# Performance work log

Measured on AMD Instinct MI355X. Metric: run time of the kernel, lower is better.

The kernel has to match this reference:

```python
import jax, jax.numpy as jnp
import numpy as np

B, N, C, K = 2, 4096, 256, 64


def setup_inputs() -> dict:
    key = jax.random.key(0)
    k1, k2, k3, k4, k5, k6 = jax.random.split(key, 6)
    points = jax.random.normal(k1, (B, N, 3), dtype=jnp.float32)  # ~N(0,1) cloud
    point_features = jax.random.normal(k2, (B, N, C), dtype=jnp.float32)
    # proposals: centers inside the cloud, positive box dims, random yaw (unused by mask math)
    centers = jax.random.uniform(k3, (B, K, 3), minval=-1.0, maxval=1.0, dtype=jnp.float32)
    dims = jax.random.uniform(k4, (B, K, 3), minval=0.5, maxval=1.5, dtype=jnp.float32)
    ry = jax.random.uniform(k5, (B, K, 1), minval=-np.pi, maxval=np.pi, dtype=jnp.float32)
    proposals = jnp.concatenate([centers, dims, ry], axis=-1)  # (B,K,7)
    W1 = jax.random.normal(k6, (C, 256), dtype=jnp.float32) * (1.0 / np.sqrt(C))
    b1 = jnp.zeros((256,), dtype=jnp.float32)
    W2 = jax.random.normal(jax.random.fold_in(key, 7), (256, 256), dtype=jnp.float32) * (1.0 / 16.0)
    b2 = jnp.zeros((256,), dtype=jnp.float32)
    return {"points": points, "point_features": point_features, "proposals": proposals,
            "W1": W1, "b1": b1, "W2": W2, "b2": b2}


def reference(points, point_features, proposals, W1, b1, W2, b2):
    # points: (B,N,3), point_features: (B,N,C), proposals: (B,K,7)
    ctr = proposals[..., :3]                      # (B,K,3) cx,cy,cz
    half = proposals[..., 3:6] * 0.5              # (B,K,3) l/2,w/2,h/2
    lo = ctr - half                               # (B,K,3)
    hi = ctr + half
    # point-in-box mask (axis-aligned, strict inequalities as in source): (B,K,N)
    p = points[:, None, :, :]                     # (B,1,N,3)
    mask = jnp.all((p > lo[:, :, None, :]) & (p < hi[:, :, None, :]), axis=-1)
    any_in = jnp.any(mask, axis=-1)               # (B,K)
    # masked max-pool over points: (B,K,N,C) -> (B,K,C)
    neg_inf = jnp.asarray(-jnp.inf, point_features.dtype)
    masked = jnp.where(mask[..., None], point_features[:, None, :, :], neg_inf)
    pooled = jnp.max(masked, axis=2)
    pooled = jnp.where(any_in[..., None], pooled, 0.0)  # empty box -> zeros
    # fc: Linear(C,256) + ReLU + Linear(256,256) + ReLU
    h = jax.nn.relu(jnp.einsum('bkc,cd->bkd', pooled, W1) + b1)
    out = jax.nn.relu(jnp.einsum('bkd,de->bke', h, W2) + b2)
    return out
```

## Files before the change

kernel.cpp:

```cpp
#include <hip/hip_runtime.h>

#define Bn 2
#define Nn 4096
#define Cn 256
#define Kn 64
#define BK (Bn * Kn)
#define NW 16
#define BT 1024

__device__ __forceinline__ float4 max4(float4 a, float4 b) {
    return make_float4(fmaxf(a.x, b.x), fmaxf(a.y, b.y),
                       fmaxf(a.z, b.z), fmaxf(a.w, b.w));
}

__global__ __launch_bounds__(BT) void fused_roi_kernel(
    const float* __restrict__ points,
    const float* __restrict__ feats,
    const float* __restrict__ proposals,
    const float* __restrict__ W1,
    const float* __restrict__ b1,
    const float* __restrict__ W2,
    const float* __restrict__ b2,
    float* __restrict__ out)
{
    const int bk   = blockIdx.x;
    const int b    = bk / Kn;
    const int tid  = threadIdx.x;
    const int w    = tid >> 6;
    const int lane = tid & 63;

    __shared__ int   s_idx[Nn];
    __shared__ int   s_count;
    __shared__ float s_part[NW][Cn];
    __shared__ float s_vec[Cn];
    __shared__ float s_red[4][Cn];

    const float* prop = proposals + (size_t)bk * 7;
    const float cx = prop[0], cy = prop[1], cz = prop[2];
    const float hx = prop[3] * 0.5f, hy = prop[4] * 0.5f, hz = prop[5] * 0.5f;
    const float lox = cx - hx, loy = cy - hy, loz = cz - hz;
    const float hix = cx + hx, hiy = cy + hy, hiz = cz + hz;

    if (tid == 0) s_count = 0;
    __syncthreads();

    const float* pts = points + (size_t)b * Nn * 3;
    #pragma unroll
    for (int n = tid; n < Nn; n += BT) {
        const float px = pts[n * 3 + 0];
        const float py = pts[n * 3 + 1];
        const float pz = pts[n * 3 + 2];
        const bool in = (px > lox) & (px < hix) &
                        (py > loy) & (py < hiy) &
                        (pz > loz) & (pz < hiz);
        if (in) {
            const int pos = atomicAdd(&s_count, 1);
            s_idx[pos] = n;
        }
    }
    __syncthreads();
    const int count = s_count;

    const float* fb = feats + (size_t)b * Nn * Cn;
    float4 mx = make_float4(-INFINITY, -INFINITY, -INFINITY, -INFINITY);
    int i = w;
    for (; i + 7 * NW < count; i += 8 * NW) {
        const int a0 = s_idx[i + 0 * NW], a1 = s_idx[i + 1 * NW];
        const int a2 = s_idx[i + 2 * NW], a3 = s_idx[i + 3 * NW];
        const int a4 = s_idx[i + 4 * NW], a5 = s_idx[i + 5 * NW];
        const int a6 = s_idx[i + 6 * NW], a7 = s_idx[i + 7 * NW];
        const float4 f0 = *(const float4*)(fb + (size_t)a0 * Cn + lane * 4);
        const float4 f1 = *(const float4*)(fb + (size_t)a1 * Cn + lane * 4);
        const float4 f2 = *(const float4*)(fb + (size_t)a2 * Cn + lane * 4);
        const float4 f3 = *(const float4*)(fb + (size_t)a3 * Cn + lane * 4);
        const float4 f4 = *(const float4*)(fb + (size_t)a4 * Cn + lane * 4);
        const float4 f5 = *(const float4*)(fb + (size_t)a5 * Cn + lane * 4);
        const float4 f6 = *(const float4*)(fb + (size_t)a6 * Cn + lane * 4);
        const float4 f7 = *(const float4*)(fb + (size_t)a7 * Cn + lane * 4);
        mx = max4(mx, max4(max4(f0, f1), max4(f2, f3)));
        mx = max4(mx, max4(max4(f4, f5), max4(f6, f7)));
    }
    for (; i < count; i += NW) {
        const int a = s_idx[i];
        mx = max4(mx, *(const float4*)(fb + (size_t)a * Cn + lane * 4));
    }
    *(float4*)&s_part[w][lane * 4] = mx;
    __syncthreads();

    if (tid < Cn) {
        float m = s_part[0][tid];
        #pragma unroll
        for (int k = 1; k < NW; ++k) m = fmaxf(m, s_part[k][tid]);
        if (m == -INFINITY) m = 0.0f;
        s_vec[tid] = m;
    }
    __syncthreads();

    {
        const int g = tid >> 8;
        const int d = tid & 255;
        const float* w1 = W1 + (size_t)(g * 64) * 256 + d;
        const float* sv = s_vec + g * 64;
        float acc = 0.0f;
        #pragma unroll 16
        for (int c = 0; c < 64; ++c) {
            acc = fmaf(sv[c], w1[(size_t)c * 256], acc);
        }
        s_red[g][d] = acc;
    }
    __syncthreads();
    if (tid < Cn) {
        const float h = fmaxf(
            b1[tid] + ((s_red[0][tid] + s_red[1][tid]) +
                       (s_red[2][tid] + s_red[3][tid])), 0.0f);
        s_vec[tid] = h;
    }
    __syncthreads();

    {
        const int g = tid >> 8;
        const int d = tid & 255;
        const float* w2 = W2 + (size_t)(g * 64) * 256 + d;
        const float* sv = s_vec + g * 64;
        float acc = 0.0f;
        #pragma unroll 16
        for (int c = 0; c < 64; ++c) {
            acc = fmaf(sv[c], w2[(size_t)c * 256], acc);
        }
        s_red[g][d] = acc;
    }
    __syncthreads();
    if (tid < Cn) {
        out[(size_t)bk * 256 + tid] = fmaxf(
            b2[tid] + ((s_red[0][tid] + s_red[1][tid]) +
                       (s_red[2][tid] + s_red[3][tid])), 0.0f);
    }
}

extern "C" void kernel_launch(void* const* d_in, const int* in_sizes, int n_in,
                              void* d_out, int out_size, void* d_ws, size_t ws_size,
                              hipStream_t stream) {
    const float* points    = (const float*)d_in[0];
    const float* feats     = (const float*)d_in[1];
    const float* proposals = (const float*)d_in[2];
    const float* W1        = (const float*)d_in[3];
    const float* b1        = (const float*)d_in[4];
    const float* W2        = (const float*)d_in[5];
    const float* b2        = (const float*)d_in[6];
    float* out             = (float*)d_out;
    (void)d_ws; (void)ws_size;

    fused_roi_kernel<<<BK, BT, 0, stream>>>(points, feats, proposals,
                                            W1, b1, W2, b2, out);
}
```

Baseline: 82.21 us.

## Stream features once per chunk and scatter max into all boxes via LDS atomics

Pooling changes from per-box gathering, where each of the 128 blocks re-reads the features of its in-box points, to a point-major pass. 64 blocks each load a 128-row chunk of features once, test it against all 64 boxes with a wave ballot, and apply order-preserving unsigned atomicMax into a shared 64x256 accumulator. Partial maxima go to workspace, and a second kernel reduces the 32 chunks and runs the MLP. This removes redundant global feature reads across overlapping boxes, but adds a second launch, a 4 MB workspace round trip, and many serialized LDS atomics.

```diff
diff --git a/kernel.cpp b/kernel.cpp
--- a/kernel.cpp
+++ b/kernel.cpp
@@ -5,129 +5,150 @@
 #define Cn 256
 #define Kn 64
 #define BK (Bn * Kn)
-#define NW 16
-#define BT 1024
+#define CHUNKS 32
+#define CROWS (Nn / CHUNKS)
+#define NBLK1 (Bn * CHUNKS)
 
-__device__ __forceinline__ float4 max4(float4 a, float4 b) {
-    return make_float4(fmaxf(a.x, b.x), fmaxf(a.y, b.y),
-                       fmaxf(a.z, b.z), fmaxf(a.w, b.w));
+__device__ __forceinline__ unsigned enc_f32(float x) {
+    const unsigned b = __float_as_uint(x);
+    return (b & 0x80000000u) ? ~b : (b | 0x80000000u);
+}
+__device__ __forceinline__ float dec_f32(unsigned e) {
+    return __uint_as_float((e & 0x80000000u) ? (e & 0x7FFFFFFFu) : ~e);
 }
 
-__global__ __launch_bounds__(BT) void fused_roi_kernel(
+__global__ __launch_bounds__(1024) void pool_stream_kernel(
     const float* __restrict__ points,
     const float* __restrict__ feats,
     const float* __restrict__ proposals,
+    unsigned* __restrict__ partial)
+{
+    const int blk   = blockIdx.x;
+    const int b     = blk >> 5;
+    const int chunk = blk & (CHUNKS - 1);
+    const int tid   = threadIdx.x;
+    const int w     = tid >> 6;
+    const int lane  = tid & 63;
+    const int base  = chunk * CROWS;
+
+    __shared__ unsigned s_acc[Kn * Cn];
+    __shared__ float    s_pts[CROWS * 3];
+
+    #pragma unroll
+    for (int i = tid; i < Kn * Cn; i += 1024) s_acc[i] = 0u;
+    if (tid < CROWS * 3)
+        s_pts[tid] = points[(size_t)b * Nn * 3 + base * 3 + tid];
+
+    const float* prop = proposals + ((size_t)b * Kn + lane) * 7;
+    const float cx = prop[0], cy = prop[1], cz = prop[2];
+    const float hx = prop[3] * 0.5f, hy = prop[4] * 0.5f, hz = prop[5] * 0.5f;
+    const float lox = cx - hx, loy = cy - hy, loz = cz - hz;
+    const float hix = cx + hx, hiy = cy + hy, hiz = cz + hz;
+    __syncthreads();
+
+    const float* fb = feats + (size_t)b * Nn * Cn;
+    float f[8][4];
+    #pragma unroll
+    for (int j = 0; j < 8; ++j) {
+        const size_t r = (size_t)(base + w + 16 * j) * Cn;
+        #pragma unroll
+        for (int c = 0; c < 4; ++c)
+            f[j][c] = fb[r + c * 64 + lane];
+    }
+
+    #pragma unroll
+    for (int j = 0; j < 8; ++j) {
+        const int lr = w + 16 * j;
+        const float px = s_pts[lr * 3 + 0];
+        const float py = s_pts[lr * 3 + 1];
+        const float pz = s_pts[lr * 3 + 2];
+        const bool in = (px > lox) & (px < hix) &
+                        (py > loy) & (py < hiy) &
+                        (pz > loz) & (pz < hiz);
+        unsigned long long mask = __ballot(in);
+        if (mask) {
+            const unsigned e0 = enc_f32(f[j][0]);
+            const unsigned e1 = enc_f32(f[j][1]);
+            const unsigned e2 = enc_f32(f[j][2]);
+            const unsigned e3 = enc_f32(f[j][3]);
+            while (mask) {
+                const int k = (int)__builtin_ctzll(mask);
+                mask &= mask - 1;
+                atomicMax(&s_acc[k * Cn +   0 + lane], e0);
+                atomicMax(&s_acc[k * Cn +  64 + lane], e1);
+                atomicMax(&s_acc[k * Cn + 128 + lane], e2);
+                atomicMax(&s_acc[k * Cn + 192 + lane], e3);
+            }
+        }
+    }
+    __syncthreads();
+
+    uint4* po = (uint4*)(partial + (size_t)blk * Kn * Cn);
+    const uint4* pa = (const uint4*)s_acc;
+    #pragma unroll
+    for (int i = tid; i < Kn * Cn / 4; i += 1024) po[i] = pa[i];
+}
+
+__global__ __launch_bounds__(1024) void reduce_mlp_kernel(
+    const unsigned* __restrict__ partial,
     const float* __restrict__ W1,
     const float* __restrict__ b1,
     const float* __restrict__ W2,
     const float* __restrict__ b2,
     float* __restrict__ out)
 {
-    const int bk   = blockIdx.x;
-    const int b    = bk / Kn;
-    const int tid  = threadIdx.x;
-    const int w    = tid >> 6;
-    const int lane = tid & 63;
+    const int bk  = blockIdx.x;
+    const int b   = bk >> 6;
+    const int k   = bk & 63;
+    const int tid = threadIdx.x;
+    const int g   = tid >> 8;
+    const int ch  = tid & 255;
 
-    __shared__ int   s_idx[Nn];
-    __shared__ int   s_count;
-    __shared__ float s_part[NW][Cn];
-    __shared__ float s_vec[Cn];
-    __shared__ float s_red[4][Cn];
+    __shared__ unsigned s_m[4][Cn];
+    __shared__ float    s_vec[Cn];
+    __shared__ float    s_red[4][Cn];
 
-    const float* prop = proposals + (size_t)bk * 7;
-    const float cx = prop[0], cy = prop[1], cz = prop[2];
-    const float hx = prop[3] * 0.5f, hy = prop[4] * 0.5f, hz = prop[5] * 0.5f;
-    const float lox = cx - hx, loy = cy - hy, loz = cz - hz;
-    const float hix = cx + hx, hiy = cy + hy, hiz = cz + hz;
-
-    if (tid == 0) s_count = 0;
-    __syncthreads();
-
-    const float* pts = points + (size_t)b * Nn * 3;
+    const unsigned* pp = partial +
+        ((size_t)(b * CHUNKS) * Kn + k) * Cn + ch;
+    unsigned m = 0u;
     #pragma unroll
-    for (int n = tid; n < Nn; n += BT) {
-        const float px = pts[n * 3 + 0];
-        const float py = pts[n * 3 + 1];
-        const float pz = pts[n * 3 + 2];
-        const bool in = (px > lox) & (px < hix) &
-                        (py > loy) & (py < hiy) &
-                        (pz > loz) & (pz < hiz);
-        if (in) {
-            const int pos = atomicAdd(&s_count, 1);
-            s_idx[pos] = n;
-        }
-    }
-    __syncthreads();
-    const int count = s_count;
-
-    const float* fb = feats + (size_t)b * Nn * Cn;
-    float4 mx = make_float4(-INFINITY, -INFINITY, -INFINITY, -INFINITY);
-    int i = w;
-    for (; i + 7 * NW < count; i += 8 * NW) {
-        const int a0 = s_idx[i + 0 * NW], a1 = s_idx[i + 1 * NW];
-        const int a2 = s_idx[i + 2 * NW], a3 = s_idx[i + 3 * NW];
-        const int a4 = s_idx[i + 4 * NW], a5 = s_idx[i + 5 * NW];
-        const int a6 = s_idx[i + 6 * NW], a7 = s_idx[i + 7 * NW];
-        const float4 f0 = *(const float4*)(fb + (size_t)a0 * Cn + lane * 4);
-        const float4 f1 = *(const float4*)(fb + (size_t)a1 * Cn + lane * 4);
-        const float4 f2 = *(const float4*)(fb + (size_t)a2 * Cn + lane * 4);
-        const float4 f3 = *(const float4*)(fb + (size_t)a3 * Cn + lane * 4);
-        const float4 f4 = *(const float4*)(fb + (size_t)a4 * Cn + lane * 4);
-        const float4 f5 = *(const float4*)(fb + (size_t)a5 * Cn + lane * 4);
-        const float4 f6 = *(const float4*)(fb + (size_t)a6 * Cn + lane * 4);
-        const float4 f7 = *(const float4*)(fb + (size_t)a7 * Cn + lane * 4);
-        mx = max4(mx, max4(max4(f0, f1), max4(f2, f3)));
-        mx = max4(mx, max4(max4(f4, f5), max4(f6, f7)));
-    }
-    for (; i < count; i += NW) {
-        const int a = s_idx[i];
-        mx = max4(mx, *(const float4*)(fb + (size_t)a * Cn + lane * 4));
-    }
-    *(float4*)&s_part[w][lane * 4] = mx;
+    for (int j = 0; j < 8; ++j)
+        m = max(m, pp[(size_t)(g * 8 + j) * Kn * Cn]);
+    s_m[g][ch] = m;
     __syncthreads();
 
     if (tid < Cn) {
-        float m = s_part[0][tid];
-        #pragma unroll
-        for (int k = 1; k < NW; ++k) m = fmaxf(m, s_part[k][tid]);
-        if (m == -INFINITY) m = 0.0f;
-        s_vec[tid] = m;
+        const unsigned e = max(max(s_m[0][tid], s_m[1][tid]),
+                               max(s_m[2][tid], s_m[3][tid]));
+        s_vec[tid] = (e == 0u) ? 0.0f : dec_f32(e);
     }
     __syncthreads();
 
     {
-        const int g = tid >> 8;
-        const int d = tid & 255;
-        const float* w1 = W1 + (size_t)(g * 64) * 256 + d;
+        const float* w1 = W1 + (size_t)(g * 64) * 256 + ch;
         const float* sv = s_vec + g * 64;
         float acc = 0.0f;
         #pragma unroll 16
-        for (int c = 0; c < 64; ++c) {
+        for (int c = 0; c < 64; ++c)
             acc = fmaf(sv[c], w1[(size_t)c * 256], acc);
-        }
-        s_red[g][d] = acc;
+        s_red[g][ch] = acc;
     }
     __syncthreads();
     if (tid < Cn) {
-        const float h = fmaxf(
+        s_vec[tid] = fmaxf(
             b1[tid] + ((s_red[0][tid] + s_red[1][tid]) +
                        (s_red[2][tid] + s_red[3][tid])), 0.0f);
-        s_vec[tid] = h;
     }
     __syncthreads();
 
     {
-        const int g = tid >> 8;
-        const int d = tid & 255;
-        const float* w2 = W2 + (size_t)(g * 64) * 256 + d;
+        const float* w2 = W2 + (size_t)(g * 64) * 256 + ch;
         const float* sv = s_vec + g * 64;
         float acc = 0.0f;
         #pragma unroll 16
-        for (int c = 0; c < 64; ++c) {
+        for (int c = 0; c < 64; ++c)
             acc = fmaf(sv[c], w2[(size_t)c * 256], acc);
-        }
-        s_red[g][d] = acc;
+        s_red[g][ch] = acc;
     }
     __syncthreads();
     if (tid < Cn) {
@@ -148,8 +169,9 @@
     const float* W2        = (const float*)d_in[5];
     const float* b2        = (const float*)d_in[6];
     float* out             = (float*)d_out;
-    (void)d_ws; (void)ws_size;
+    unsigned* partial      = (unsigned*)d_ws;
 
-    fused_roi_kernel<<<BK, BT, 0, stream>>>(points, feats, proposals,
-                                            W1, b1, W2, b2, out);
+    pool_stream_kernel<<<NBLK1, 1024, 0, stream>>>(points, feats, proposals,
+                                                   partial);
+    reduce_mlp_kernel<<<BK, 1024, 0, stream>>>(partial, W1, b1, W2, b2, out);
 }
```

Result: slower. 85.17 us (+3.6%).
